# Optimization experiments

Measured on AMD Instinct MI355X. Metric: run time of the kernel, lower is better.

Reference implementation:

```python
import jax, jax.numpy as jnp
import numpy as np

N_NODES = 100000
N_EDGES = 200000
N_ATOM_FEATS = 56
HIDDEN = 256
N_GRAPHS = 2048
OUT_DIM = 1
EPS = 1e-5  # torch BatchNorm1d default


def setup_inputs() -> dict:
    key = jax.random.key(0)
    ks = jax.random.split(key, 10)
    x = jax.random.randint(ks[0], (N_NODES, N_ATOM_FEATS), 0, 2, dtype=jnp.int64 if jax.config.jax_enable_x64 else jnp.int32)
    edge_index = jax.random.randint(ks[1], (2, N_EDGES), 0, N_NODES)
    batch = jnp.sort(jax.random.randint(ks[2], (N_NODES,), 0, N_GRAPHS))
    emb_tables = jax.random.normal(ks[3], (N_ATOM_FEATS, 2, HIDDEN), dtype=jnp.float32) * 0.1
    Ws = jax.random.normal(ks[4], (3, HIDDEN, HIDDEN), dtype=jnp.float32) * (1.0 / np.sqrt(HIDDEN))
    bs = jnp.zeros((3, HIDDEN), dtype=jnp.float32)
    gammas = jnp.ones((2, HIDDEN), dtype=jnp.float32)
    betas = jnp.zeros((2, HIDDEN), dtype=jnp.float32)
    lin_w = jax.random.normal(ks[5], (HIDDEN, OUT_DIM), dtype=jnp.float32) * (1.0 / np.sqrt(HIDDEN))
    lin_b = jnp.zeros((OUT_DIM,), dtype=jnp.float32)
    return {"x": x, "edge_index": edge_index, "batch": batch, "emb_tables": emb_tables,
            "Ws": Ws, "bs": bs, "gammas": gammas, "betas": betas, "lin_w": lin_w, "lin_b": lin_b}


def reference(x, edge_index, batch, emb_tables, Ws, bs, gammas, betas, lin_w, lin_b):
    n = x.shape[0]
    # --- AtomEncoder: sum of 56 per-feature embedding lookups ---
    # emb_tables: [56, 2, H]; x: [N, 56] -> gathered [N, 56, H] -> sum over feature axis
    feat_idx = jnp.arange(x.shape[1])[None, :]  # [1,56]
    h = emb_tables[feat_idx, x].sum(axis=1)      # [N, H]

    # --- GCN normalization with self-loops (shared across layers) ---
    loops = jnp.arange(n)
    src = jnp.concatenate([edge_index[0], loops])
    dst = jnp.concatenate([edge_index[1], loops])
    deg = jax.ops.segment_sum(jnp.ones_like(src, dtype=h.dtype), dst, num_segments=n)
    dinv = jnp.where(deg > 0, jax.lax.rsqrt(deg), 0.0)
    norm = dinv[src] * dinv[dst]  # [E+N]

    def gcn_conv(h, W, b):
        hw = h @ W                                   # [N, H']
        msg = hw[src] * norm[:, None]                # gather + scale
        agg = jax.ops.segment_sum(msg, dst, num_segments=n)  # scatter-add
        return agg + b

    # --- layers 0..L-2: conv -> batchnorm (batch stats) -> relu; eval => no dropout ---
    for i in range(2):
        h = gcn_conv(h, Ws[i], bs[i])
        mu = h.mean(axis=0)
        var = h.var(axis=0)
        h = (h - mu) * jax.lax.rsqrt(var + EPS) * gammas[i] + betas[i]
        h = jax.nn.relu(h)
    # --- last conv (return_embeds=True: no softmax) ---
    h = gcn_conv(h, Ws[2], bs[2])

    # --- global mean pool over graphs ---
    sums = jax.ops.segment_sum(h, batch, num_segments=N_GRAPHS)          # [G, H]
    counts = jax.ops.segment_sum(jnp.ones((n,), h.dtype), batch, num_segments=N_GRAPHS)
    pooled = sums / jnp.maximum(counts, 1.0)[:, None]

    return pooled @ lin_w + lin_b  # [G, OUT_DIM]
```

## Files before the change

### kernel.cpp

```cpp
#include <hip/hip_runtime.h>
#include <hip/hip_bf16.h>

#define NN 100000
#define NE 200000
#define NF 56
#define HD 256
#define NG 2048

#define SCAN_CH 512
#define NCH ((NN + SCAN_CH - 1) / SCAN_CH)
#define EB ((NE + 255) / 256)

#define AB 2048
#define ZB 98
#define CVB ((NN + 255) / 256)
#define ENB ((NN + 127) / 128)

typedef __bf16 bf16x8 __attribute__((ext_vector_type(8)));
typedef __bf16 bf16x4 __attribute__((ext_vector_type(4)));
typedef float  floatx4 __attribute__((ext_vector_type(4)));

__global__ void prep_params(const float* __restrict__ emb, const float* __restrict__ Ws,
                            const float* __restrict__ bs, const float* __restrict__ lw,
                            __bf16* __restrict__ dW0t,
                            float* __restrict__ w2lw, float* __restrict__ b2lw,
                            __bf16* __restrict__ Wt, unsigned* __restrict__ deg,
                            const int* __restrict__ x, __bf16* __restrict__ xb) {
    __shared__ float row[HD];
    int c = threadIdx.x;
    int f = blockIdx.x;
    if (f >= NF + 2) {
        int g = f - (NF + 2);
        if (g < HD) {
            Wt[(size_t)g * HD + c] = (__bf16)Ws[(size_t)HD * HD + (size_t)c * HD + g];
        } else if (g < HD + ZB) {
            int idx = (g - HD) * HD + c;
            if (idx < NN / 4) ((int4*)deg)[idx] = make_int4(0, 0, 0, 0);
        } else {
            int r = (g - HD - ZB) * 256 + c;
            if (r < NN) {
                const int* xr = x + (size_t)r * NF;
                __bf16 o[64];
                #pragma unroll
                for (int j = 0; j < 14; ++j) {
                    int4 iv = *(const int4*)&xr[j * 4];
                    o[j * 4 + 0] = (__bf16)(float)iv.x;
                    o[j * 4 + 1] = (__bf16)(float)iv.y;
                    o[j * 4 + 2] = (__bf16)(float)iv.z;
                    o[j * 4 + 3] = (__bf16)(float)iv.w;
                }
                o[56] = (__bf16)1.0f;
                #pragma unroll
                for (int j = 57; j < 64; ++j) o[j] = (__bf16)0.0f;
                #pragma unroll
                for (int j = 0; j < 8; ++j)
                    *(bf16x8*)&xb[(size_t)r * 64 + j * 8] = *(const bf16x8*)&o[j * 8];
            }
        }
        return;
    }
    if (f == NF + 1) {
        const float* W2 = Ws + (size_t)2 * HD * HD;
        float acc = 0.f;
        for (int k = 0; k < HD; ++k) acc += W2[(size_t)c * HD + k] * lw[k];
        w2lw[c] = acc;
        row[c] = bs[2 * HD + c] * lw[c];
        __syncthreads();
        for (int off = 128; off > 0; off >>= 1) {
            if (c < off) row[c] += row[c + off];
            __syncthreads();
        }
        if (c == 0) *b2lw = row[0];
        return;
    }
    if (f < NF) {
        row[c] = emb[(f * 2 + 1) * HD + c] - emb[(f * 2 + 0) * HD + c];
    } else {
        float s = 0.f;
        for (int ff = 0; ff < NF; ++ff) s += emb[(ff * 2) * HD + c];
        row[c] = s;
    }
    __syncthreads();
    float acc = 0.f;
    for (int k = 0; k < HD; ++k) acc += row[k] * Ws[k * HD + c];
    if (f < NF) {
        dW0t[c * 64 + f] = (__bf16)acc;
    } else {
        dW0t[c * 64 + 56] = (__bf16)acc;
        #pragma unroll
        for (int k = 57; k < 64; ++k) dW0t[c * 64 + k] = (__bf16)0.f;
    }
}

__global__ void deg_kernel(const int* __restrict__ dst, unsigned* __restrict__ deg, int E) {
    int e = blockIdx.x * blockDim.x + threadIdx.x;
    if (e < E) atomicAdd(&deg[dst[e]], 1u);
}

__global__ void chunk_sum_dinv(const unsigned* __restrict__ deg, unsigned* __restrict__ csum,
                               float* __restrict__ dinv, float* __restrict__ selfn) {
    __shared__ unsigned s[SCAN_CH];
    int t = threadIdx.x;
    int base = blockIdx.x * SCAN_CH;
    unsigned v = (base + t < NN) ? deg[base + t] : 0u;
    s[t] = v;
    if (base + t < NN) {
        float d = (float)(v + 1u);
        dinv[base + t]  = rsqrtf(d);
        selfn[base + t] = 1.0f / d;
    }
    __syncthreads();
    for (int off = SCAN_CH / 2; off > 0; off >>= 1) {
        if (t < off) s[t] += s[t + off];
        __syncthreads();
    }
    if (t == 0) csum[blockIdx.x] = s[0];
}

__global__ void chunk_apply(const unsigned* __restrict__ deg, const unsigned* __restrict__ csum,
                            unsigned* __restrict__ row_start, unsigned* __restrict__ cursor) {
    __shared__ unsigned s[SCAN_CH];
    __shared__ unsigned cs[256];
    int t = threadIdx.x;
    if (t < 256) cs[t] = (t < NCH) ? csum[t] : 0u;
    __syncthreads();
    for (int off = 1; off < 256; off <<= 1) {
        unsigned add = (t < 256 && t >= off) ? cs[t - off] : 0u;
        __syncthreads();
        if (t < 256) cs[t] += add;
        __syncthreads();
    }
    unsigned chunk_base = (blockIdx.x == 0) ? 0u : cs[blockIdx.x - 1];

    int base = blockIdx.x * SCAN_CH;
    unsigned v = (base + t < NN) ? deg[base + t] : 0u;
    s[t] = v;
    __syncthreads();
    for (int off = 1; off < SCAN_CH; off <<= 1) {
        unsigned add = (t >= off) ? s[t - off] : 0u;
        __syncthreads();
        s[t] += add;
        __syncthreads();
    }
    if (base + t < NN) {
        unsigned rs = chunk_base + s[t] - v;
        row_start[base + t] = rs;
        cursor[base + t] = rs;
    }
    if (blockIdx.x == 0 && t == 0) row_start[NN] = NE;
}

__global__ void csr_fill_gb(const int* __restrict__ src, const int* __restrict__ dst,
                            const float* __restrict__ dinv, unsigned* __restrict__ cursor,
                            int* __restrict__ ecol, float* __restrict__ enorm,
                            const int* __restrict__ batch, unsigned* __restrict__ gstart) {
    int t = threadIdx.x;
    if (blockIdx.x < EB) {
        int e = blockIdx.x * 256 + t;
        if (e < NE) {
            int s = src[e], d = dst[e];
            unsigned pos = atomicAdd(&cursor[d], 1u);
            ecol[pos] = s;
            enorm[pos] = dinv[s] * dinv[d];
        }
    } else {
        int g = (blockIdx.x - EB) * 256 + t;
        if (g <= NG) {
            int lo = 0, hi = NN;
            while (lo < hi) {
                int mid = (lo + hi) >> 1;
                if (batch[mid] < g) lo = mid + 1; else hi = mid;
            }
            gstart[g] = (unsigned)lo;
        }
    }
}

#define ELSTR 68
__global__ void __launch_bounds__(512) enc_fused(const __bf16* __restrict__ xb,
                                                 const __bf16* __restrict__ dW0t,
                                                 const float* __restrict__ b0,
                                                 const float* __restrict__ selfn,
                                                 const unsigned* __restrict__ row_start,
                                                 const int* __restrict__ ecol,
                                                 const float* __restrict__ enorm,
                                                 __bf16* __restrict__ C,
                                                 float* __restrict__ part) {
    __shared__ __bf16 sA[128 * ELSTR];
    __shared__ __bf16 sB[256 * ELSTR];
    __shared__ float psum[8][64];
    __shared__ float psq[8][64];
    int t = threadIdx.x;
    int m0 = blockIdx.x * 128;
    int lane = t & 63, w = t >> 6;
    int quad = lane >> 4, l16 = lane & 15;
    int mw = (w & 1) * 64, nw = (w >> 1) * 64;

    {
        int bn = t >> 1;
        int kh = (t & 1) * 32;
        #pragma unroll
        for (int j = 0; j < 4; ++j)
            *(bf16x8*)&sB[bn * ELSTR + kh + j * 8] =
                *(const bf16x8*)&dW0t[(size_t)bn * 64 + kh + j * 8];
    }
    {
        int r = t >> 2;
        int p = (t & 3) * 16;
        int n = m0 + r;
        float acc[16];
        #pragma unroll
        for (int i = 0; i < 16; ++i) acc[i] = 0.f;
        if (n < NN) {
            float sn = selfn[n];
            bf16x8 a0 = *(const bf16x8*)&xb[(size_t)n * 64 + p];
            bf16x8 a1 = *(const bf16x8*)&xb[(size_t)n * 64 + p + 8];
            #pragma unroll
            for (int i = 0; i < 8; ++i) {
                acc[i]     = (float)a0[i] * sn;
                acc[8 + i] = (float)a1[i] * sn;
            }
            unsigned e0 = row_start[n], e1 = row_start[n + 1];
            unsigned e = e0;
            for (; e + 2 <= e1; e += 2) {
                int s0 = ecol[e], s1 = ecol[e + 1];
                float n0v = enorm[e], n1v = enorm[e + 1];
                bf16x8 u00 = *(const bf16x8*)&xb[(size_t)s0 * 64 + p];
                bf16x8 u01 = *(const bf16x8*)&xb[(size_t)s0 * 64 + p + 8];
                bf16x8 u10 = *(const bf16x8*)&xb[(size_t)s1 * 64 + p];
                bf16x8 u11 = *(const bf16x8*)&xb[(size_t)s1 * 64 + p + 8];
                #pragma unroll
                for (int i = 0; i < 8; ++i) {
                    acc[i]     += (float)u00[i] * n0v + (float)u10[i] * n1v;
                    acc[8 + i] += (float)u01[i] * n0v + (float)u11[i] * n1v;
                }
            }
            if (e < e1) {
                int s0 = ecol[e];
                float n0v = enorm[e];
                bf16x8 u00 = *(const bf16x8*)&xb[(size_t)s0 * 64 + p];
                bf16x8 u01 = *(const bf16x8*)&xb[(size_t)s0 * 64 + p + 8];
                #pragma unroll
                for (int i = 0; i < 8; ++i) {
                    acc[i]     += (float)u00[i] * n0v;
                    acc[8 + i] += (float)u01[i] * n0v;
                }
            }
        }
        bf16x8 o0, o1;
        #pragma unroll
        for (int i = 0; i < 8; ++i) { o0[i] = (__bf16)acc[i]; o1[i] = (__bf16)acc[8 + i]; }
        *(bf16x8*)&sA[r * ELSTR + p]     = o0;
        *(bf16x8*)&sA[r * ELSTR + p + 8] = o1;
    }
    __syncthreads();

    floatx4 acc[4][4] = {};
    #pragma unroll
    for (int s = 0; s < 2; ++s) {
        bf16x8 af[4], bfr[4];
        #pragma unroll
        for (int i = 0; i < 4; ++i)
            af[i] = *(const bf16x8*)&sA[(mw + i * 16 + l16) * ELSTR + s * 32 + quad * 8];
        #pragma unroll
        for (int i = 0; i < 4; ++i)
            bfr[i] = *(const bf16x8*)&sB[(nw + i * 16 + l16) * ELSTR + s * 32 + quad * 8];
        #pragma unroll
        for (int mi = 0; mi < 4; ++mi)
            #pragma unroll
            for (int ni = 0; ni < 4; ++ni)
                acc[mi][ni] = __builtin_amdgcn_mfma_f32_16x16x32_bf16(
                    af[mi], bfr[ni], acc[mi][ni], 0, 0, 0);
    }

    float bw[4];
    #pragma unroll
    for (int ni = 0; ni < 4; ++ni) bw[ni] = b0[nw + ni * 16 + l16];
    float ls[4] = {0.f, 0.f, 0.f, 0.f};
    float lq[4] = {0.f, 0.f, 0.f, 0.f};
    #pragma unroll
    for (int mi = 0; mi < 4; ++mi) {
        #pragma unroll
        for (int r = 0; r < 4; ++r) {
            int row = m0 + mw + mi * 16 + quad * 4 + r;
            if (row < NN) {
                #pragma unroll
                for (int ni = 0; ni < 4; ++ni) {
                    float v = acc[mi][ni][r] + bw[ni];
                    C[(size_t)row * HD + nw + ni * 16 + l16] = (__bf16)v;
                    ls[ni] += v;
                    lq[ni] += v * v;
                }
            }
        }
    }
    #pragma unroll
    for (int ni = 0; ni < 4; ++ni) {
        ls[ni] += __shfl_xor(ls[ni], 16, 64);
        ls[ni] += __shfl_xor(ls[ni], 32, 64);
        lq[ni] += __shfl_xor(lq[ni], 16, 64);
        lq[ni] += __shfl_xor(lq[ni], 32, 64);
    }
    if (lane < 16) {
        #pragma unroll
        for (int ni = 0; ni < 4; ++ni) {
            psum[w][ni * 16 + l16] = ls[ni];
            psq[w][ni * 16 + l16]  = lq[ni];
        }
    }
    __syncthreads();
    if (!(w & 1) && lane < 16) {
        #pragma unroll
        for (int ni = 0; ni < 4; ++ni) {
            int ci = ni * 16 + l16;
            part[(size_t)blockIdx.x * 512 + nw + ci]       = psum[w][ci] + psum[w + 1][ci];
            part[(size_t)blockIdx.x * 512 + 256 + nw + ci] = psq[w][ci]  + psq[w + 1][ci];
        }
    }
}

#define LSTR 36
__global__ void __launch_bounds__(512) gemm_mfma(const __bf16* __restrict__ A,
                                                 const __bf16* __restrict__ Wt,
                                                 __bf16* __restrict__ C, int M,
                                                 const float* __restrict__ ascale,
                                                 const float* __restrict__ ashift) {
    __shared__ __bf16 sA[128 * LSTR];
    __shared__ __bf16 sB[256 * LSTR];
    int t = threadIdx.x;
    int m0 = blockIdx.x * 128;
    int lane = t & 63, w = t >> 6;
    int quad = lane >> 4, l16 = lane & 15;
    int mw = (w & 1) * 64;
    int nw = (w >> 1) * 64;

    int ar = t >> 2;
    int ak = (t & 3) * 8;
    int bn = t >> 1;
    int bk = (t & 1) * 16;

    auto ldA = [&](int k0, bf16x8& pa) {
        float4 s0 = *(const float4*)&ascale[k0 + ak];
        float4 s1 = *(const float4*)&ascale[k0 + ak + 4];
        float4 h0 = *(const float4*)&ashift[k0 + ak];
        float4 h1 = *(const float4*)&ashift[k0 + ak + 4];
        int row = m0 + ar;
        bf16x8 a = {};
        if (row < M) a = *(const bf16x8*)&A[(size_t)row * HD + k0 + ak];
        bf16x8 b;
        b[0] = (__bf16)fmaxf((float)a[0] * s0.x + h0.x, 0.f);
        b[1] = (__bf16)fmaxf((float)a[1] * s0.y + h0.y, 0.f);
        b[2] = (__bf16)fmaxf((float)a[2] * s0.z + h0.z, 0.f);
        b[3] = (__bf16)fmaxf((float)a[3] * s0.w + h0.w, 0.f);
        b[4] = (__bf16)fmaxf((float)a[4] * s1.x + h1.x, 0.f);
        b[5] = (__bf16)fmaxf((float)a[5] * s1.y + h1.y, 0.f);
        b[6] = (__bf16)fmaxf((float)a[6] * s1.z + h1.z, 0.f);
        b[7] = (__bf16)fmaxf((float)a[7] * s1.w + h1.w, 0.f);
        pa = b;
    };
    auto ldB = [&](int k0, bf16x8 pb[2]) {
        #pragma unroll
        for (int j = 0; j < 2; ++j)
            pb[j] = *(const bf16x8*)&Wt[(size_t)bn * HD + k0 + bk + j * 8];
    };

    bf16x8 pa, pb[2];
    ldA(0, pa);
    ldB(0, pb);

    floatx4 acc[4][4] = {};

    for (int k0 = 0; k0 < 256; k0 += 32) {
        *(bf16x8*)&sA[ar * LSTR + ak] = pa;
        *(bf16x8*)&sB[bn * LSTR + bk]     = pb[0];
        *(bf16x8*)&sB[bn * LSTR + bk + 8] = pb[1];
        __syncthreads();

        if (k0 + 32 < 256) {
            ldA(k0 + 32, pa);
            ldB(k0 + 32, pb);
        }

        bf16x8 af[4], bfr[4];
        #pragma unroll
        for (int i = 0; i < 4; ++i)
            af[i] = *(const bf16x8*)&sA[(mw + i * 16 + l16) * LSTR + quad * 8];
        #pragma unroll
        for (int i = 0; i < 4; ++i)
            bfr[i] = *(const bf16x8*)&sB[(nw + i * 16 + l16) * LSTR + quad * 8];
        #pragma unroll
        for (int mi = 0; mi < 4; ++mi)
            #pragma unroll
            for (int ni = 0; ni < 4; ++ni)
                acc[mi][ni] = __builtin_amdgcn_mfma_f32_16x16x32_bf16(
                    af[mi], bfr[ni], acc[mi][ni], 0, 0, 0);
        __syncthreads();
    }

    #pragma unroll
    for (int mi = 0; mi < 4; ++mi) {
        #pragma unroll
        for (int r = 0; r < 4; ++r) {
            int row = m0 + mw + mi * 16 + quad * 4 + r;
            if (row < M) {
                #pragma unroll
                for (int ni = 0; ni < 4; ++ni)
                    C[(size_t)row * HD + nw + ni * 16 + l16] = (__bf16)acc[mi][ni][r];
            }
        }
    }
}

__global__ void __launch_bounds__(256) gcn_aggregate(const __bf16* __restrict__ hw,
                                                     const float* __restrict__ selfn,
                                                     const float* __restrict__ bias,
                                                     const unsigned* __restrict__ row_start,
                                                     const int* __restrict__ ecol,
                                                     const float* __restrict__ enorm,
                                                     __bf16* __restrict__ agg,
                                                     float* __restrict__ part) {
    int t = threadIdx.x;
    int l = t & 63, w = t >> 6;
    int c4 = l * 4;
    float4 bv = *(const float4*)&bias[c4];
    float4 lsum = make_float4(0.f, 0.f, 0.f, 0.f);
    float4 lssq = make_float4(0.f, 0.f, 0.f, 0.f);

    for (int n = blockIdx.x * 4 + w; n < NN; n += AB * 4) {
        float s = selfn[n];
        bf16x4 hv = *(const bf16x4*)&hw[(size_t)n * HD + c4];
        float4 acc;
        acc.x = (float)hv[0] * s + bv.x;
        acc.y = (float)hv[1] * s + bv.y;
        acc.z = (float)hv[2] * s + bv.z;
        acc.w = (float)hv[3] * s + bv.w;
        unsigned e0 = row_start[n], e1 = row_start[n + 1];
        unsigned e = e0;
        for (; e + 4 <= e1; e += 4) {
            int sv0 = ecol[e], sv1 = ecol[e + 1], sv2 = ecol[e + 2], sv3 = ecol[e + 3];
            float nm0 = enorm[e], nm1 = enorm[e + 1], nm2 = enorm[e + 2], nm3 = enorm[e + 3];
            bf16x4 u0 = *(const bf16x4*)&hw[(size_t)sv0 * HD + c4];
            bf16x4 u1 = *(const bf16x4*)&hw[(size_t)sv1 * HD + c4];
            bf16x4 u2 = *(const bf16x4*)&hw[(size_t)sv2 * HD + c4];
            bf16x4 u3 = *(const bf16x4*)&hw[(size_t)sv3 * HD + c4];
            acc.x += (float)u0[0] * nm0 + (float)u1[0] * nm1 + (float)u2[0] * nm2 + (float)u3[0] * nm3;
            acc.y += (float)u0[1] * nm0 + (float)u1[1] * nm1 + (float)u2[1] * nm2 + (float)u3[1] * nm3;
            acc.z += (float)u0[2] * nm0 + (float)u1[2] * nm1 + (float)u2[2] * nm2 + (float)u3[2] * nm3;
            acc.w += (float)u0[3] * nm0 + (float)u1[3] * nm1 + (float)u2[3] * nm2 + (float)u3[3] * nm3;
        }
        for (; e + 2 <= e1; e += 2) {
            int sv0 = ecol[e], sv1 = ecol[e + 1];
            float nm0 = enorm[e], nm1 = enorm[e + 1];
            bf16x4 u0 = *(const bf16x4*)&hw[(size_t)sv0 * HD + c4];
            bf16x4 u1 = *(const bf16x4*)&hw[(size_t)sv1 * HD + c4];
            acc.x += (float)u0[0] * nm0 + (float)u1[0] * nm1;
            acc.y += (float)u0[1] * nm0 + (float)u1[1] * nm1;
            acc.z += (float)u0[2] * nm0 + (float)u1[2] * nm1;
            acc.w += (float)u0[3] * nm0 + (float)u1[3] * nm1;
        }
        if (e < e1) {
            int sv = ecol[e];
            float nm = enorm[e];
            bf16x4 u = *(const bf16x4*)&hw[(size_t)sv * HD + c4];
            acc.x += (float)u[0] * nm;
            acc.y += (float)u[1] * nm;
            acc.z += (float)u[2] * nm;
            acc.w += (float)u[3] * nm;
        }
        bf16x4 o;
        o[0] = (__bf16)acc.x; o[1] = (__bf16)acc.y;
        o[2] = (__bf16)acc.z; o[3] = (__bf16)acc.w;
        *(bf16x4*)&agg[(size_t)n * HD + c4] = o;

        lsum.x += acc.x; lsum.y += acc.y; lsum.z += acc.z; lsum.w += acc.w;
        lssq.x += acc.x * acc.x; lssq.y += acc.y * acc.y;
        lssq.z += acc.z * acc.z; lssq.w += acc.w * acc.w;
    }

    __shared__ float4 ssum[4][64];
    __shared__ float4 sss[4][64];
    ssum[w][l] = lsum;
    sss[w][l]  = lssq;
    __syncthreads();
    if (w == 0) {
        float4 a0 = ssum[0][l], a1 = ssum[1][l], a2 = ssum[2][l], a3 = ssum[3][l];
        float4 q0 = sss[0][l],  q1 = sss[1][l],  q2 = sss[2][l],  q3 = sss[3][l];
        float4 sm, sq;
        sm.x = a0.x + a1.x + a2.x + a3.x;
        sm.y = a0.y + a1.y + a2.y + a3.y;
        sm.z = a0.z + a1.z + a2.z + a3.z;
        sm.w = a0.w + a1.w + a2.w + a3.w;
        sq.x = q0.x + q1.x + q2.x + q3.x;
        sq.y = q0.y + q1.y + q2.y + q3.y;
        sq.z = q0.z + q1.z + q2.z + q3.z;
        sq.w = q0.w + q1.w + q2.w + q3.w;
        *(float4*)&part[(size_t)blockIdx.x * 512 + c4]       = sm;
        *(float4*)&part[(size_t)blockIdx.x * 512 + 256 + c4] = sq;
    }
}

__global__ void __launch_bounds__(256) bn_scale(const float* __restrict__ part, int nb,
                                                const float* __restrict__ gamma,
                                                const float* __restrict__ beta,
                                                float* __restrict__ scale,
                                                float* __restrict__ shift) {
    __shared__ float rs[256], rq[256];
    int t = threadIdx.x;
    int c = blockIdx.x;
    float s = 0.f, q = 0.f;
    for (int j = t; j < nb; j += 256) {
        s += part[(size_t)j * 512 + c];
        q += part[(size_t)j * 512 + 256 + c];
    }
    rs[t] = s; rq[t] = q;
    __syncthreads();
    for (int off = 128; off > 0; off >>= 1) {
        if (t < off) { rs[t] += rs[t + off]; rq[t] += rq[t + off]; }
        __syncthreads();
    }
    if (t == 0) {
        const float inv_n = 1.0f / (float)NN;
        float mu  = rs[0] * inv_n;
        float var = rq[0] * inv_n - mu * mu;
        float rstd = rsqrtf(var + 1e-5f);
        float sc = gamma[c] * rstd;
        scale[c] = sc;
        shift[c] = beta[c] - mu * sc;
    }
}

__global__ void __launch_bounds__(256) bn_dot(const __bf16* __restrict__ h,
                                              const float* __restrict__ scale,
                                              const float* __restrict__ shift,
                                              const float* __restrict__ w2lw,
                                              float* __restrict__ z) {
    int tid = blockIdx.x * 256 + threadIdx.x;
    int n = tid >> 6;
    if (n >= NN) return;
    int l = tid & 63;
    int c4 = l * 4;
    bf16x4 a = *(const bf16x4*)&h[(size_t)n * HD + c4];
    float4 sc = *(const float4*)&scale[c4];
    float4 sh = *(const float4*)&shift[c4];
    float4 wv = *(const float4*)&w2lw[c4];
    float d = fmaxf((float)a[0] * sc.x + sh.x, 0.f) * wv.x
            + fmaxf((float)a[1] * sc.y + sh.y, 0.f) * wv.y
            + fmaxf((float)a[2] * sc.z + sh.z, 0.f) * wv.z
            + fmaxf((float)a[3] * sc.w + sh.w, 0.f) * wv.w;
    #pragma unroll
    for (int off = 32; off > 0; off >>= 1) d += __shfl_down(d, off, 64);
    if (l == 0) z[n] = d;
}

__global__ void __launch_bounds__(256) pool_fused(const float* __restrict__ z,
                                                  const float* __restrict__ selfn,
                                                  const float* __restrict__ b2lw,
                                                  const unsigned* __restrict__ row_start,
                                                  const int* __restrict__ ecol,
                                                  const float* __restrict__ enorm,
                                                  const unsigned* __restrict__ gstart,
                                                  const float* __restrict__ lb,
                                                  float* __restrict__ out) {
    int tid = blockIdx.x * 256 + threadIdx.x;
    int g = tid >> 6;
    if (g >= NG) return;
    int l = tid & 63;
    unsigned s0 = gstart[g], s1 = gstart[g + 1];
    float bb = *b2lw;
    float s = 0.f;
    for (unsigned i = s0 + l; i < s1; i += 64) {
        float d = selfn[i] * z[i] + bb;
        unsigned e0 = row_start[i], e1 = row_start[i + 1];
        for (unsigned e = e0; e < e1; ++e)
            d += enorm[e] * z[ecol[e]];
        s += d;
    }
    #pragma unroll
    for (int off = 32; off > 0; off >>= 1) s += __shfl_down(s, off, 64);
    if (l == 0) out[g] = s / fmaxf((float)(s1 - s0), 1.0f) + lb[0];
}

extern "C" void kernel_launch(void* const* d_in, const int* in_sizes, int n_in,
                              void* d_out, int out_size, void* d_ws, size_t ws_size,
                              hipStream_t stream) {
    const int*   x     = (const int*)d_in[0];
    const int*   ei    = (const int*)d_in[1];
    const int*   batch = (const int*)d_in[2];
    const float* emb   = (const float*)d_in[3];
    const float* Ws    = (const float*)d_in[4];
    const float* bs    = (const float*)d_in[5];
    const float* gam   = (const float*)d_in[6];
    const float* bet   = (const float*)d_in[7];
    const float* lw    = (const float*)d_in[8];
    const float* lb    = (const float*)d_in[9];
    float* out = (float*)d_out;

    const int* src = ei;
    const int* dst = ei + NE;

    char* p = (char*)d_ws;
    size_t off = 0;
    auto carve = [&](size_t bytes) { void* r = p + off; off = (off + bytes + 255) & ~(size_t)255; return r; };
    __bf16*   buf0   = (__bf16*)carve((size_t)NN * HD * 2);
    __bf16*   buf1   = (__bf16*)carve((size_t)NN * HD * 2);
    __bf16*   xb     = (__bf16*)carve((size_t)NN * 64 * 2);
    __bf16*   dW0t   = (__bf16*)carve(HD * 64 * 2);
    __bf16*   Wt     = (__bf16*)carve((size_t)HD * HD * 2);
    float*    w2lw   = (float*)carve(HD * 4);
    float*    b2lw   = (float*)carve(256);
    unsigned* deg    = (unsigned*)carve(NN * 4);
    float*    dinv   = (float*)carve(NN * 4);
    float*    selfn  = (float*)carve(NN * 4);
    unsigned* csum   = (unsigned*)carve(256 * 4);
    unsigned* row_s  = (unsigned*)carve((NN + 1) * 4);
    unsigned* cursor = (unsigned*)carve(NN * 4);
    int*      ecol   = (int*)carve(NE * 4);
    float*    enorm  = (float*)carve(NE * 4);
    float*    part   = (float*)carve((size_t)AB * 512 * 4);
    float*    scale  = (float*)carve(HD * 4);
    float*    shift  = (float*)carve(HD * 4);
    unsigned* gstart = (unsigned*)carve((NG + 1) * 4);
    float*    zbuf   = (float*)carve(NN * 4);
    (void)ws_size; (void)n_in; (void)in_sizes; (void)out_size;

    prep_params<<<NF + 2 + HD + ZB + CVB, HD, 0, stream>>>(
        emb, Ws, bs, lw, dW0t, w2lw, b2lw, Wt, deg, x, xb);

    deg_kernel<<<(NE + 255) / 256, 256, 0, stream>>>(dst, deg, NE);
    chunk_sum_dinv<<<NCH, SCAN_CH, 0, stream>>>(deg, csum, dinv, selfn);
    chunk_apply<<<NCH, SCAN_CH, 0, stream>>>(deg, csum, row_s, cursor);
    csr_fill_gb<<<EB + (NG + 256) / 256, 256, 0, stream>>>(
        src, dst, dinv, cursor, ecol, enorm, batch, gstart);

    enc_fused<<<ENB, 512, 0, stream>>>(
        xb, dW0t, bs, selfn, row_s, ecol, enorm, buf0, part);
    bn_scale<<<HD, 256, 0, stream>>>(part, ENB, gam, bet, scale, shift);

    gemm_mfma<<<ENB, 512, 0, stream>>>(buf0, Wt, buf1, NN, scale, shift);
    gcn_aggregate<<<AB, 256, 0, stream>>>(
        buf1, selfn, bs + HD, row_s, ecol, enorm, buf0, part);
    bn_scale<<<HD, 256, 0, stream>>>(part, AB, gam + HD, bet + HD, scale, shift);

    bn_dot<<<(NN * 64 + 255) / 256, 256, 0, stream>>>(buf0, scale, shift, w2lw, zbuf);
    pool_fused<<<(NG * 64 + 255) / 256, 256, 0, stream>>>(
        zbuf, selfn, b2lw, row_s, ecol, enorm, gstart, lb, out);
}
```

Baseline: 253.3 us.

## Fuse layer-1 aggregation into GEMM by aggregating before multiplying

```diff
diff --git a/kernel.cpp b/kernel.cpp
--- a/kernel.cpp
+++ b/kernel.cpp
@@ -11,10 +11,10 @@
 #define NCH ((NN + SCAN_CH - 1) / SCAN_CH)
 #define EB ((NE + 255) / 256)
 
-#define AB 2048
 #define ZB 98
 #define CVB ((NN + 255) / 256)
 #define ENB ((NN + 127) / 128)
+#define GNB ((NN + 63) / 64)
 
 typedef __bf16 bf16x8 __attribute__((ext_vector_type(8)));
 typedef __bf16 bf16x4 __attribute__((ext_vector_type(4)));
@@ -319,183 +319,143 @@
     }
 }
 
-#define LSTR 36
-__global__ void __launch_bounds__(512) gemm_mfma(const __bf16* __restrict__ A,
+__global__ void __launch_bounds__(512) gcn_fused(const __bf16* __restrict__ h0,
+                                                 const float* __restrict__ scale,
+                                                 const float* __restrict__ shift,
                                                  const __bf16* __restrict__ Wt,
-                                                 __bf16* __restrict__ C, int M,
-                                                 const float* __restrict__ ascale,
-                                                 const float* __restrict__ ashift) {
-    __shared__ __bf16 sA[128 * LSTR];
-    __shared__ __bf16 sB[256 * LSTR];
+                                                 const float* __restrict__ b1,
+                                                 const float* __restrict__ selfn,
+                                                 const unsigned* __restrict__ row_start,
+                                                 const int* __restrict__ ecol,
+                                                 const float* __restrict__ enorm,
+                                                 __bf16* __restrict__ C,
+                                                 float* __restrict__ part) {
+    __shared__ __bf16 sA[64 * 256];
+    __shared__ __bf16 sB[256 * 36];
     int t = threadIdx.x;
-    int m0 = blockIdx.x * 128;
+    int m0 = blockIdx.x * 64;
     int lane = t & 63, w = t >> 6;
     int quad = lane >> 4, l16 = lane & 15;
-    int mw = (w & 1) * 64;
-    int nw = (w >> 1) * 64;
-
-    int ar = t >> 2;
-    int ak = (t & 3) * 8;
-    int bn = t >> 1;
-    int bk = (t & 1) * 16;
-
-    auto ldA = [&](int k0, bf16x8& pa) {
-        float4 s0 = *(const float4*)&ascale[k0 + ak];
-        float4 s1 = *(const float4*)&ascale[k0 + ak + 4];
-        float4 h0 = *(const float4*)&ashift[k0 + ak];
-        float4 h1 = *(const float4*)&ashift[k0 + ak + 4];
-        int row = m0 + ar;
-        bf16x8 a = {};
-        if (row < M) a = *(const bf16x8*)&A[(size_t)row * HD + k0 + ak];
-        bf16x8 b;
-        b[0] = (__bf16)fmaxf((float)a[0] * s0.x + h0.x, 0.f);
-        b[1] = (__bf16)fmaxf((float)a[1] * s0.y + h0.y, 0.f);
-        b[2] = (__bf16)fmaxf((float)a[2] * s0.z + h0.z, 0.f);
-        b[3] = (__bf16)fmaxf((float)a[3] * s0.w + h0.w, 0.f);
-        b[4] = (__bf16)fmaxf((float)a[4] * s1.x + h1.x, 0.f);
-        b[5] = (__bf16)fmaxf((float)a[5] * s1.y + h1.y, 0.f);
-        b[6] = (__bf16)fmaxf((float)a[6] * s1.z + h1.z, 0.f);
-        b[7] = (__bf16)fmaxf((float)a[7] * s1.w + h1.w, 0.f);
-        pa = b;
-    };
-    auto ldB = [&](int k0, bf16x8 pb[2]) {
-        #pragma unroll
-        for (int j = 0; j < 2; ++j)
-            pb[j] = *(const bf16x8*)&Wt[(size_t)bn * HD + k0 + bk + j * 8];
-    };
-
-    bf16x8 pa, pb[2];
-    ldA(0, pa);
-    ldB(0, pb);
-
-    floatx4 acc[4][4] = {};
-
+
+    int bn = t >> 1, bk = (t & 1) * 16;
+    bf16x8 pb[2];
+    #pragma unroll
+    for (int j = 0; j < 2; ++j)
+        pb[j] = *(const bf16x8*)&Wt[(size_t)bn * HD + bk + j * 8];
+
+    {
+        int c4 = lane * 4;
+        float4 sc = *(const float4*)&scale[c4];
+        float4 sh = *(const float4*)&shift[c4];
+        for (int g = 0; g < 8; ++g) {
+            int r = w * 8 + g;
+            int n = m0 + r;
+            float4 acc = make_float4(0.f, 0.f, 0.f, 0.f);
+            if (n < NN) {
+                float sn = selfn[n];
+                bf16x4 hv = *(const bf16x4*)&h0[(size_t)n * HD + c4];
+                acc.x = fmaxf((float)hv[0] * sc.x + sh.x, 0.f) * sn;
+                acc.y = fmaxf((float)hv[1] * sc.y + sh.y, 0.f) * sn;
+                acc.z = fmaxf((float)hv[2] * sc.z + sh.z, 0.f) * sn;
+                acc.w = fmaxf((float)hv[3] * sc.w + sh.w, 0.f) * sn;
+                unsigned e = row_start[n], e1 = row_start[n + 1];
+                for (; e + 2 <= e1; e += 2) {
+                    int s0 = ecol[e], s1 = ecol[e + 1];
+                    float n0 = enorm[e], n1 = enorm[e + 1];
+                    bf16x4 u0 = *(const bf16x4*)&h0[(size_t)s0 * HD + c4];
+                    bf16x4 u1 = *(const bf16x4*)&h0[(size_t)s1 * HD + c4];
+                    acc.x += fmaxf((float)u0[0] * sc.x + sh.x, 0.f) * n0
+                           + fmaxf((float)u1[0] * sc.x + sh.x, 0.f) * n1;
+                    acc.y += fmaxf((float)u0[1] * sc.y + sh.y, 0.f) * n0
+                           + fmaxf((float)u1[1] * sc.y + sh.y, 0.f) * n1;
+                    acc.z += fmaxf((float)u0[2] * sc.z + sh.z, 0.f) * n0
+                           + fmaxf((float)u1[2] * sc.z + sh.z, 0.f) * n1;
+                    acc.w += fmaxf((float)u0[3] * sc.w + sh.w, 0.f) * n0
+                           + fmaxf((float)u1[3] * sc.w + sh.w, 0.f) * n1;
+                }
+                if (e < e1) {
+                    int s0 = ecol[e];
+                    float n0 = enorm[e];
+                    bf16x4 u0 = *(const bf16x4*)&h0[(size_t)s0 * HD + c4];
+                    acc.x += fmaxf((float)u0[0] * sc.x + sh.x, 0.f) * n0;
+                    acc.y += fmaxf((float)u0[1] * sc.y + sh.y, 0.f) * n0;
+                    acc.z += fmaxf((float)u0[2] * sc.z + sh.z, 0.f) * n0;
+                    acc.w += fmaxf((float)u0[3] * sc.w + sh.w, 0.f) * n0;
+                }
+            }
+            bf16x4 o;
+            o[0] = (__bf16)acc.x; o[1] = (__bf16)acc.y;
+            o[2] = (__bf16)acc.z; o[3] = (__bf16)acc.w;
+            int swz = ((lane >> 1) ^ (r & 7));
+            *(bf16x4*)&sA[r * 256 + swz * 8 + (lane & 1) * 4] = o;
+        }
+    }
+
+    floatx4 cacc[4][2] = {};
     for (int k0 = 0; k0 < 256; k0 += 32) {
-        *(bf16x8*)&sA[ar * LSTR + ak] = pa;
-        *(bf16x8*)&sB[bn * LSTR + bk]     = pb[0];
-        *(bf16x8*)&sB[bn * LSTR + bk + 8] = pb[1];
+        *(bf16x8*)&sB[bn * 36 + bk]     = pb[0];
+        *(bf16x8*)&sB[bn * 36 + bk + 8] = pb[1];
         __syncthreads();
 
         if (k0 + 32 < 256) {
-            ldA(k0 + 32, pa);
-            ldB(k0 + 32, pb);
-        }
-
-        bf16x8 af[4], bfr[4];
-        #pragma unroll
-        for (int i = 0; i < 4; ++i)
-            af[i] = *(const bf16x8*)&sA[(mw + i * 16 + l16) * LSTR + quad * 8];
-        #pragma unroll
-        for (int i = 0; i < 4; ++i)
-            bfr[i] = *(const bf16x8*)&sB[(nw + i * 16 + l16) * LSTR + quad * 8];
+            #pragma unroll
+            for (int j = 0; j < 2; ++j)
+                pb[j] = *(const bf16x8*)&Wt[(size_t)bn * HD + k0 + 32 + bk + j * 8];
+        }
+
+        bf16x8 af[4], bfr[2];
+        int gbase = (k0 >> 3) + quad;
+        #pragma unroll
+        for (int mi = 0; mi < 4; ++mi) {
+            int row = mi * 16 + l16;
+            af[mi] = *(const bf16x8*)&sA[row * 256 + ((gbase ^ (l16 & 7)) << 3)];
+        }
+        #pragma unroll
+        for (int ni = 0; ni < 2; ++ni)
+            bfr[ni] = *(const bf16x8*)&sB[(w * 32 + ni * 16 + l16) * 36 + quad * 8];
         #pragma unroll
         for (int mi = 0; mi < 4; ++mi)
             #pragma unroll
-            for (int ni = 0; ni < 4; ++ni)
-                acc[mi][ni] = __builtin_amdgcn_mfma_f32_16x16x32_bf16(
-                    af[mi], bfr[ni], acc[mi][ni], 0, 0, 0);
-        __syncthreads();
-    }
-
+            for (int ni = 0; ni < 2; ++ni)
+                cacc[mi][ni] = __builtin_amdgcn_mfma_f32_16x16x32_bf16(
+                    af[mi], bfr[ni], cacc[mi][ni], 0, 0, 0);
+        __syncthreads();
+    }
+
+    float bw[2];
+    #pragma unroll
+    for (int ni = 0; ni < 2; ++ni) bw[ni] = b1[w * 32 + ni * 16 + l16];
+    float ls[2] = {0.f, 0.f}, lq[2] = {0.f, 0.f};
     #pragma unroll
     for (int mi = 0; mi < 4; ++mi) {
         #pragma unroll
-        for (int r = 0; r < 4; ++r) {
-            int row = m0 + mw + mi * 16 + quad * 4 + r;
-            if (row < M) {
+        for (int r_ = 0; r_ < 4; ++r_) {
+            int row = m0 + mi * 16 + quad * 4 + r_;
+            if (row < NN) {
                 #pragma unroll
-                for (int ni = 0; ni < 4; ++ni)
-                    C[(size_t)row * HD + nw + ni * 16 + l16] = (__bf16)acc[mi][ni][r];
-            }
-        }
-    }
-}
-
-__global__ void __launch_bounds__(256) gcn_aggregate(const __bf16* __restrict__ hw,
-                                                     const float* __restrict__ selfn,
-                                                     const float* __restrict__ bias,
-                                                     const unsigned* __restrict__ row_start,
-                                                     const int* __restrict__ ecol,
-                                                     const float* __restrict__ enorm,
-                                                     __bf16* __restrict__ agg,
-                                                     float* __restrict__ part) {
-    int t = threadIdx.x;
-    int l = t & 63, w = t >> 6;
-    int c4 = l * 4;
-    float4 bv = *(const float4*)&bias[c4];
-    float4 lsum = make_float4(0.f, 0.f, 0.f, 0.f);
-    float4 lssq = make_float4(0.f, 0.f, 0.f, 0.f);
-
-    for (int n = blockIdx.x * 4 + w; n < NN; n += AB * 4) {
-        float s = selfn[n];
-        bf16x4 hv = *(const bf16x4*)&hw[(size_t)n * HD + c4];
-        float4 acc;
-        acc.x = (float)hv[0] * s + bv.x;
-        acc.y = (float)hv[1] * s + bv.y;
-        acc.z = (float)hv[2] * s + bv.z;
-        acc.w = (float)hv[3] * s + bv.w;
-        unsigned e0 = row_start[n], e1 = row_start[n + 1];
-        unsigned e = e0;
-        for (; e + 4 <= e1; e += 4) {
-            int sv0 = ecol[e], sv1 = ecol[e + 1], sv2 = ecol[e + 2], sv3 = ecol[e + 3];
-            float nm0 = enorm[e], nm1 = enorm[e + 1], nm2 = enorm[e + 2], nm3 = enorm[e + 3];
-            bf16x4 u0 = *(const bf16x4*)&hw[(size_t)sv0 * HD + c4];
-            bf16x4 u1 = *(const bf16x4*)&hw[(size_t)sv1 * HD + c4];
-            bf16x4 u2 = *(const bf16x4*)&hw[(size_t)sv2 * HD + c4];
-            bf16x4 u3 = *(const bf16x4*)&hw[(size_t)sv3 * HD + c4];
-            acc.x += (float)u0[0] * nm0 + (float)u1[0] * nm1 + (float)u2[0] * nm2 + (float)u3[0] * nm3;
-            acc.y += (float)u0[1] * nm0 + (float)u1[1] * nm1 + (float)u2[1] * nm2 + (float)u3[1] * nm3;
-            acc.z += (float)u0[2] * nm0 + (float)u1[2] * nm1 + (float)u2[2] * nm2 + (float)u3[2] * nm3;
-            acc.w += (float)u0[3] * nm0 + (float)u1[3] * nm1 + (float)u2[3] * nm2 + (float)u3[3] * nm3;
-        }
-        for (; e + 2 <= e1; e += 2) {
-            int sv0 = ecol[e], sv1 = ecol[e + 1];
-            float nm0 = enorm[e], nm1 = enorm[e + 1];
-            bf16x4 u0 = *(const bf16x4*)&hw[(size_t)sv0 * HD + c4];
-            bf16x4 u1 = *(const bf16x4*)&hw[(size_t)sv1 * HD + c4];
-            acc.x += (float)u0[0] * nm0 + (float)u1[0] * nm1;
-            acc.y += (float)u0[1] * nm0 + (float)u1[1] * nm1;
-            acc.z += (float)u0[2] * nm0 + (float)u1[2] * nm1;
-            acc.w += (float)u0[3] * nm0 + (float)u1[3] * nm1;
-        }
-        if (e < e1) {
-            int sv = ecol[e];
-            float nm = enorm[e];
-            bf16x4 u = *(const bf16x4*)&hw[(size_t)sv * HD + c4];
-            acc.x += (float)u[0] * nm;
-            acc.y += (float)u[1] * nm;
-            acc.z += (float)u[2] * nm;
-            acc.w += (float)u[3] * nm;
-        }
-        bf16x4 o;
-        o[0] = (__bf16)acc.x; o[1] = (__bf16)acc.y;
-        o[2] = (__bf16)acc.z; o[3] = (__bf16)acc.w;
-        *(bf16x4*)&agg[(size_t)n * HD + c4] = o;
-
-        lsum.x += acc.x; lsum.y += acc.y; lsum.z += acc.z; lsum.w += acc.w;
-        lssq.x += acc.x * acc.x; lssq.y += acc.y * acc.y;
-        lssq.z += acc.z * acc.z; lssq.w += acc.w * acc.w;
-    }
-
-    __shared__ float4 ssum[4][64];
-    __shared__ float4 sss[4][64];
-    ssum[w][l] = lsum;
-    sss[w][l]  = lssq;
-    __syncthreads();
-    if (w == 0) {
-        float4 a0 = ssum[0][l], a1 = ssum[1][l], a2 = ssum[2][l], a3 = ssum[3][l];
-        float4 q0 = sss[0][l],  q1 = sss[1][l],  q2 = sss[2][l],  q3 = sss[3][l];
-        float4 sm, sq;
-        sm.x = a0.x + a1.x + a2.x + a3.x;
-        sm.y = a0.y + a1.y + a2.y + a3.y;
-        sm.z = a0.z + a1.z + a2.z + a3.z;
-        sm.w = a0.w + a1.w + a2.w + a3.w;
-        sq.x = q0.x + q1.x + q2.x + q3.x;
-        sq.y = q0.y + q1.y + q2.y + q3.y;
-        sq.z = q0.z + q1.z + q2.z + q3.z;
-        sq.w = q0.w + q1.w + q2.w + q3.w;
-        *(float4*)&part[(size_t)blockIdx.x * 512 + c4]       = sm;
-        *(float4*)&part[(size_t)blockIdx.x * 512 + 256 + c4] = sq;
+                for (int ni = 0; ni < 2; ++ni) {
+                    float v = cacc[mi][ni][r_] + bw[ni];
+                    C[(size_t)row * HD + w * 32 + ni * 16 + l16] = (__bf16)v;
+                    ls[ni] += v;
+                    lq[ni] += v * v;
+                }
+            }
+        }
+    }
+    #pragma unroll
+    for (int ni = 0; ni < 2; ++ni) {
+        ls[ni] += __shfl_xor(ls[ni], 16, 64);
+        ls[ni] += __shfl_xor(ls[ni], 32, 64);
+        lq[ni] += __shfl_xor(lq[ni], 16, 64);
+        lq[ni] += __shfl_xor(lq[ni], 32, 64);
+    }
+    if (lane < 16) {
+        #pragma unroll
+        for (int ni = 0; ni < 2; ++ni) {
+            int ci = w * 32 + ni * 16 + l16;
+            part[(size_t)blockIdx.x * 512 + ci]       = ls[ni];
+            part[(size_t)blockIdx.x * 512 + 256 + ci] = lq[ni];
+        }
     }
 }
 
@@ -616,7 +576,7 @@
     unsigned* cursor = (unsigned*)carve(NN * 4);
     int*      ecol   = (int*)carve(NE * 4);
     float*    enorm  = (float*)carve(NE * 4);
-    float*    part   = (float*)carve((size_t)AB * 512 * 4);
+    float*    part   = (float*)carve((size_t)GNB * 512 * 4);
     float*    scale  = (float*)carve(HD * 4);
     float*    shift  = (float*)carve(HD * 4);
     unsigned* gstart = (unsigned*)carve((NG + 1) * 4);
@@ -636,12 +596,11 @@
         xb, dW0t, bs, selfn, row_s, ecol, enorm, buf0, part);
     bn_scale<<<HD, 256, 0, stream>>>(part, ENB, gam, bet, scale, shift);
 
-    gemm_mfma<<<ENB, 512, 0, stream>>>(buf0, Wt, buf1, NN, scale, shift);
-    gcn_aggregate<<<AB, 256, 0, stream>>>(
-        buf1, selfn, bs + HD, row_s, ecol, enorm, buf0, part);
-    bn_scale<<<HD, 256, 0, stream>>>(part, AB, gam + HD, bet + HD, scale, shift);
-
-    bn_dot<<<(NN * 64 + 255) / 256, 256, 0, stream>>>(buf0, scale, shift, w2lw, zbuf);
+    gcn_fused<<<GNB, 512, 0, stream>>>(
+        buf0, scale, shift, Wt, bs + HD, selfn, row_s, ecol, enorm, buf1, part);
+    bn_scale<<<HD, 256, 0, stream>>>(part, GNB, gam + HD, bet + HD, scale, shift);
+
+    bn_dot<<<(NN * 64 + 255) / 256, 256, 0, stream>>>(buf1, scale, shift, w2lw, zbuf);
     pool_fused<<<(NG * 64 + 255) / 256, 256, 0, stream>>>(
         zbuf, selfn, b2lw, row_s, ecol, enorm, gstart, lb, out);
 }
```

Measured after the change: 248.7 us, median of 2. Within noise of the previous version (-1.8%).
